# Performance work log

Hardware: AMD Instinct MI355X
Metric: run time of the kernel (lower is better)

## Reference

```python
import jax, jax.numpy as jnp
import numpy as np

H = 64  # hidden_size
IN = 1  # input_size
OUT = 7  # output_size
B, T = 4096, 512


def setup_inputs() -> dict:
    key = jax.random.key(0)
    ks = jax.random.split(key, 11)
    s = 1.0 / np.sqrt(H)  # PyTorch LSTM init scale
    u = lambda k, shp: jax.random.uniform(k, shp, jnp.float32, -s, s)
    return {
        "x": jax.random.normal(ks[0], (B, T, IN), jnp.float32),
        # layer 0
        "Wih0": u(ks[1], (4 * H, IN)),
        "Whh0": u(ks[2], (4 * H, H)),
        "bih0": u(ks[3], (4 * H,)),
        "bhh0": u(ks[4], (4 * H,)),
        # layer 1
        "Wih1": u(ks[5], (4 * H, H)),
        "Whh1": u(ks[6], (4 * H, H)),
        "bih1": u(ks[7], (4 * H,)),
        "bhh1": u(ks[8], (4 * H,)),
        # fc head
        "Wfc": u(ks[9], (OUT, H)),
        "bfc": u(ks[10], (OUT,)),
    }


def _lstm_layer(x, Wih, Whh, bih, bhh):
    """x: [B, T, F] -> hidden sequence [B, T, H]. PyTorch gate order i,f,g,o."""
    b, t, _ = x.shape
    h = Whh.shape[1]
    # precompute input contribution for all timesteps: [T, B, 4H]
    xg = (jnp.einsum('btf,gf->btg', x, Wih) + bih + bhh).transpose(1, 0, 2)
    WhhT = Whh.T  # [H, 4H]

    def step(carry, g_t):
        h_t, c_t = carry
        gates = g_t + h_t @ WhhT  # [B, 4H]
        i, f, g, o = jnp.split(gates, 4, axis=-1)
        i = jax.nn.sigmoid(i)
        f = jax.nn.sigmoid(f)
        g = jnp.tanh(g)
        o = jax.nn.sigmoid(o)
        c_new = f * c_t + i * g
        h_new = o * jnp.tanh(c_new)
        return (h_new, c_new), h_new

    h0 = jnp.zeros((b, h), x.dtype)
    c0 = jnp.zeros((b, h), x.dtype)
    (_, _), hs = jax.lax.scan(step, (h0, c0), xg)
    return hs.transpose(1, 0, 2)  # [B, T, H]


def reference(x, Wih0, Whh0, bih0, bhh0, Wih1, Whh1, bih1, bhh1, Wfc, bfc):
    h1 = _lstm_layer(x, Wih0, Whh0, bih0, bhh0)   # dropout between layers is identity in eval
    h2 = _lstm_layer(h1, Wih1, Whh1, bih1, bhh1)
    last = h2[:, -1, :]  # [B, H]; dropout identity in eval
    return last @ Wfc.T + bfc  # [B, OUT]
```

## Files before the change

kernel.cpp:

```cpp
#include <hip/hip_runtime.h>

#define HH 64
#define TT 512
#define BB 16

typedef __attribute__((ext_vector_type(8))) short short8;
typedef __attribute__((ext_vector_type(4))) float f32x4;

static __device__ __forceinline__ unsigned short f2bf(float f) {
  unsigned u = __float_as_uint(f);
  u += 0x7fffu + ((u >> 16) & 1u);
  return (unsigned short)(u >> 16);
}

static __device__ __forceinline__ float sigm(float x) {
  float e = __builtin_amdgcn_exp2f(-1.442695041f * x);
  return __builtin_amdgcn_rcpf(1.0f + e);
}
static __device__ __forceinline__ float tanh_fast(float x) {
  float e = __builtin_amdgcn_exp2f(2.885390082f * x);
  return 1.0f - 2.0f * __builtin_amdgcn_rcpf(1.0f + e);
}

static __device__ __forceinline__ short8 pack8(const float* __restrict__ p) {
  const float4* p4 = (const float4*)p;
  float4 a = p4[0], b = p4[1];
  short8 r;
  r[0] = (short)f2bf(a.x); r[1] = (short)f2bf(a.y);
  r[2] = (short)f2bf(a.z); r[3] = (short)f2bf(a.w);
  r[4] = (short)f2bf(b.x); r[5] = (short)f2bf(b.y);
  r[6] = (short)f2bf(b.z); r[7] = (short)f2bf(b.w);
  return r;
}

static __device__ __forceinline__ short8 ldfrag(const unsigned short* buf, int m, int q, int kt) {
  const int off = (kt * 64 + q * 16) ^ ((m & 7) << 4);
  return *(const short8*)((const char*)buf + m * 128 + off);
}

__global__ __launch_bounds__(512)
void lstm2_fused(const float* __restrict__ x,
                 const float* __restrict__ Wih0, const float* __restrict__ Whh0,
                 const float* __restrict__ bih0, const float* __restrict__ bhh0,
                 const float* __restrict__ Wih1, const float* __restrict__ Whh1,
                 const float* __restrict__ bih1, const float* __restrict__ bhh1,
                 const float* __restrict__ Wfc,  const float* __restrict__ bfc,
                 float* __restrict__ out)
{
  __shared__ float xs[TT * BB];
  __shared__ __align__(16) unsigned short h0buf[BB * HH];
  __shared__ __align__(16) unsigned short h1buf[BB * HH];
  __shared__ float h1f[BB * HH];

  const int tid  = threadIdx.x;
  const int wave = tid >> 6;
  const int lane = tid & 63;
  const int grp  = wave >> 2;
  const int w    = wave & 3;
  const int m    = lane & 15;
  const int q    = lane >> 4;
  const int b0   = blockIdx.x * BB;

  {
    const int t = tid;
    #pragma unroll
    for (int r = 0; r < BB; ++r)
      xs[t * BB + r] = x[(size_t)(b0 + r) * TT + t];
  }
  h0buf[tid] = 0; h0buf[tid + 512] = 0;
  h1buf[tid] = 0; h1buf[tid + 512] = 0;

  short8 wf[16];
  float bsum[4], wx[4];
  #pragma unroll
  for (int n = 0; n < 4; ++n) {
    const int colg = 16 * (4 * n + w) + m;
    if (grp == 0) {
      bsum[n] = bih0[colg] + bhh0[colg];
      wx[n]   = Wih0[colg];
      #pragma unroll
      for (int kt = 0; kt < 2; ++kt)
        wf[n * 2 + kt] = pack8(Whh0 + colg * HH + kt * 32 + q * 8);
    } else {
      bsum[n] = bih1[colg] + bhh1[colg];
      wx[n]   = 0.f;
      #pragma unroll
      for (int kt = 0; kt < 4; ++kt) {
        const float* Wsrc = (kt < 2) ? Wih1 : Whh1;
        wf[n * 4 + kt] = pack8(Wsrc + colg * HH + (kt & 1) * 32 + q * 8);
      }
    }
  }

  __syncthreads();

  float cst[4] = {0.f, 0.f, 0.f, 0.f};
  const int colw = 16 * w + m;

  for (int t = 0; t <= TT; ++t) {
    const bool actA = (grp == 0) && (t < TT);
    const bool actB = (grp == 1) && (t >= 1);
    short8 af0, af1, af2, af3;
    if (actA) {
      af0 = ldfrag(h0buf, m, q, 0);
      af1 = ldfrag(h0buf, m, q, 1);
    } else if (actB) {
      af0 = ldfrag(h0buf, m, q, 0);
      af1 = ldfrag(h0buf, m, q, 1);
      af2 = ldfrag(h1buf, m, q, 0);
      af3 = ldfrag(h1buf, m, q, 1);
    }
    __syncthreads();

    if (actA) {
      f32x4 acc[4];
      float xv[4];
      #pragma unroll
      for (int j = 0; j < 4; ++j) xv[j] = xs[t * BB + q * 4 + j];
      #pragma unroll
      for (int n = 0; n < 4; ++n) {
        #pragma unroll
        for (int j = 0; j < 4; ++j) acc[n][j] = fmaf(xv[j], wx[n], bsum[n]);
      }
      #pragma unroll
      for (int n = 0; n < 4; ++n) {
        acc[n] = __builtin_amdgcn_mfma_f32_16x16x32_bf16(af0, wf[n*2+0], acc[n], 0, 0, 0);
        acc[n] = __builtin_amdgcn_mfma_f32_16x16x32_bf16(af1, wf[n*2+1], acc[n], 0, 0, 0);
      }
      #pragma unroll
      for (int j = 0; j < 4; ++j) {
        float iv = sigm(acc[0][j]);
        float fv = sigm(acc[1][j]);
        float gv = tanh_fast(acc[2][j]);
        float ov = sigm(acc[3][j]);
        float c  = fmaf(fv, cst[j], iv * gv);
        cst[j] = c;
        float h  = ov * tanh_fast(c);
        const int row = q * 4 + j;
        const int off = (2 * colw) ^ ((row & 7) << 4);
        *(unsigned short*)((char*)h0buf + row * 128 + off) = f2bf(h);
      }
    } else if (actB) {
      f32x4 acc[4];
      #pragma unroll
      for (int n = 0; n < 4; ++n) {
        acc[n][0] = bsum[n]; acc[n][1] = bsum[n]; acc[n][2] = bsum[n]; acc[n][3] = bsum[n];
      }
      #pragma unroll
      for (int n = 0; n < 4; ++n) {
        acc[n] = __builtin_amdgcn_mfma_f32_16x16x32_bf16(af0, wf[n*4+0], acc[n], 0, 0, 0);
        acc[n] = __builtin_amdgcn_mfma_f32_16x16x32_bf16(af1, wf[n*4+1], acc[n], 0, 0, 0);
        acc[n] = __builtin_amdgcn_mfma_f32_16x16x32_bf16(af2, wf[n*4+2], acc[n], 0, 0, 0);
        acc[n] = __builtin_amdgcn_mfma_f32_16x16x32_bf16(af3, wf[n*4+3], acc[n], 0, 0, 0);
      }
      const bool last = (t == TT);
      #pragma unroll
      for (int j = 0; j < 4; ++j) {
        float iv = sigm(acc[0][j]);
        float fv = sigm(acc[1][j]);
        float gv = tanh_fast(acc[2][j]);
        float ov = sigm(acc[3][j]);
        float c  = fmaf(fv, cst[j], iv * gv);
        cst[j] = c;
        float h  = ov * tanh_fast(c);
        const int row = q * 4 + j;
        const int off = (2 * colw) ^ ((row & 7) << 4);
        *(unsigned short*)((char*)h1buf + row * 128 + off) = f2bf(h);
        if (last) h1f[row * HH + colw] = h;
      }
    }
    __syncthreads();
  }

  if (tid < BB * 7) {
    const int b = tid / 7, o = tid % 7;
    float s = bfc[o];
    #pragma unroll
    for (int k = 0; k < HH; ++k) s = fmaf(h1f[b * HH + k], Wfc[o * HH + k], s);
    out[(size_t)(b0 + b) * 7 + o] = s;
  }
}

extern "C" void kernel_launch(void* const* d_in, const int* in_sizes, int n_in,
                              void* d_out, int out_size, void* d_ws, size_t ws_size,
                              hipStream_t stream) {
  const float* x    = (const float*)d_in[0];
  const float* Wih0 = (const float*)d_in[1];
  const float* Whh0 = (const float*)d_in[2];
  const float* bih0 = (const float*)d_in[3];
  const float* bhh0 = (const float*)d_in[4];
  const float* Wih1 = (const float*)d_in[5];
  const float* Whh1 = (const float*)d_in[6];
  const float* bih1 = (const float*)d_in[7];
  const float* bhh1 = (const float*)d_in[8];
  const float* Wfc  = (const float*)d_in[9];
  const float* bfc  = (const float*)d_in[10];
  float* out = (float*)d_out;

  dim3 grid(4096 / BB);
  dim3 block(512);
  hipLaunchKernelGGL(lstm2_fused, grid, block, 0, stream,
                     x, Wih0, Whh0, bih0, bhh0, Wih1, Whh1, bih1, bhh1, Wfc, bfc, out);
}
```

Measured before the change: 421.8 us.

## Double the waves per block and double-buffer hidden state to drop a barrier

```diff
diff --git a/kernel.cpp b/kernel.cpp
--- a/kernel.cpp
+++ b/kernel.cpp
@@ -38,7 +38,7 @@
   return *(const short8*)((const char*)buf + m * 128 + off);
 }
 
-__global__ __launch_bounds__(512)
+__global__ __launch_bounds__(1024)
 void lstm2_fused(const float* __restrict__ x,
                  const float* __restrict__ Wih0, const float* __restrict__ Whh0,
                  const float* __restrict__ bih0, const float* __restrict__ bhh0,
@@ -48,27 +48,29 @@
                  float* __restrict__ out)
 {
   __shared__ float xs[TT * BB];
-  __shared__ __align__(16) unsigned short h0buf[BB * HH];
-  __shared__ __align__(16) unsigned short h1buf[BB * HH];
+  __shared__ __align__(16) unsigned short h0buf[2][BB * HH];
+  __shared__ __align__(16) unsigned short h1buf[2][BB * HH];
   __shared__ float h1f[BB * HH];
 
   const int tid  = threadIdx.x;
   const int wave = tid >> 6;
   const int lane = tid & 63;
-  const int grp  = wave >> 2;
-  const int w    = wave & 3;
+  const int grp  = wave >> 3;
+  const int sub  = wave & 7;
+  const int w    = sub >> 1;
+  const int jh   = sub & 1;
   const int m    = lane & 15;
   const int q    = lane >> 4;
   const int b0   = blockIdx.x * BB;
 
-  {
+  if (tid < TT) {
     const int t = tid;
     #pragma unroll
     for (int r = 0; r < BB; ++r)
       xs[t * BB + r] = x[(size_t)(b0 + r) * TT + t];
   }
-  h0buf[tid] = 0; h0buf[tid + 512] = 0;
-  h1buf[tid] = 0; h1buf[tid + 512] = 0;
+  h0buf[0][tid] = 0; h0buf[1][tid] = 0;
+  h1buf[0][tid] = 0; h1buf[1][tid] = 0;
 
   short8 wf[16];
   float bsum[4], wx[4];
@@ -94,33 +96,26 @@
 
   __syncthreads();
 
-  float cst[4] = {0.f, 0.f, 0.f, 0.f};
-  const int colw = 16 * w + m;
+  float cst[2] = {0.f, 0.f};
+  const int colw  = 16 * w + m;
+  const int jbase = 2 * jh;
 
   for (int t = 0; t <= TT; ++t) {
+    const int p = t & 1;
+    const unsigned short* h0rd = h0buf[p ^ 1];
+    const unsigned short* h1rd = h1buf[p];
+    unsigned short* h0wr = h0buf[p];
+    unsigned short* h1wr = h1buf[p ^ 1];
     const bool actA = (grp == 0) && (t < TT);
     const bool actB = (grp == 1) && (t >= 1);
-    short8 af0, af1, af2, af3;
+
     if (actA) {
-      af0 = ldfrag(h0buf, m, q, 0);
-      af1 = ldfrag(h0buf, m, q, 1);
-    } else if (actB) {
-      af0 = ldfrag(h0buf, m, q, 0);
-      af1 = ldfrag(h0buf, m, q, 1);
-      af2 = ldfrag(h1buf, m, q, 0);
-      af3 = ldfrag(h1buf, m, q, 1);
-    }
-    __syncthreads();
-
-    if (actA) {
+      short8 af0 = ldfrag(h0rd, m, q, 0);
+      short8 af1 = ldfrag(h0rd, m, q, 1);
       f32x4 acc[4];
-      float xv[4];
-      #pragma unroll
-      for (int j = 0; j < 4; ++j) xv[j] = xs[t * BB + q * 4 + j];
-      #pragma unroll
-      for (int n = 0; n < 4; ++n) {
-        #pragma unroll
-        for (int j = 0; j < 4; ++j) acc[n][j] = fmaf(xv[j], wx[n], bsum[n]);
+      #pragma unroll
+      for (int n = 0; n < 4; ++n) {
+        acc[n][0] = bsum[n]; acc[n][1] = bsum[n]; acc[n][2] = bsum[n]; acc[n][3] = bsum[n];
       }
       #pragma unroll
       for (int n = 0; n < 4; ++n) {
@@ -128,19 +123,32 @@
         acc[n] = __builtin_amdgcn_mfma_f32_16x16x32_bf16(af1, wf[n*2+1], acc[n], 0, 0, 0);
       }
       #pragma unroll
-      for (int j = 0; j < 4; ++j) {
-        float iv = sigm(acc[0][j]);
-        float fv = sigm(acc[1][j]);
-        float gv = tanh_fast(acc[2][j]);
-        float ov = sigm(acc[3][j]);
-        float c  = fmaf(fv, cst[j], iv * gv);
-        cst[j] = c;
+      for (int jj = 0; jj < 2; ++jj) {
+        float pi = jh ? acc[0][2 + jj] : acc[0][jj];
+        float pf = jh ? acc[1][2 + jj] : acc[1][jj];
+        float pg = jh ? acc[2][2 + jj] : acc[2][jj];
+        float po = jh ? acc[3][2 + jj] : acc[3][jj];
+        const float xv = xs[t * BB + q * 4 + jbase + jj];
+        pi = fmaf(xv, wx[0], pi);
+        pf = fmaf(xv, wx[1], pf);
+        pg = fmaf(xv, wx[2], pg);
+        po = fmaf(xv, wx[3], po);
+        float iv = sigm(pi);
+        float fv = sigm(pf);
+        float gv = tanh_fast(pg);
+        float ov = sigm(po);
+        float c  = fmaf(fv, cst[jj], iv * gv);
+        cst[jj] = c;
         float h  = ov * tanh_fast(c);
-        const int row = q * 4 + j;
+        const int row = q * 4 + jbase + jj;
         const int off = (2 * colw) ^ ((row & 7) << 4);
-        *(unsigned short*)((char*)h0buf + row * 128 + off) = f2bf(h);
+        *(unsigned short*)((char*)h0wr + row * 128 + off) = f2bf(h);
       }
     } else if (actB) {
+      short8 af0 = ldfrag(h0rd, m, q, 0);
+      short8 af1 = ldfrag(h0rd, m, q, 1);
+      short8 af2 = ldfrag(h1rd, m, q, 0);
+      short8 af3 = ldfrag(h1rd, m, q, 1);
       f32x4 acc[4];
       #pragma unroll
       for (int n = 0; n < 4; ++n) {
@@ -155,17 +163,21 @@
       }
       const bool last = (t == TT);
       #pragma unroll
-      for (int j = 0; j < 4; ++j) {
-        float iv = sigm(acc[0][j]);
-        float fv = sigm(acc[1][j]);
-        float gv = tanh_fast(acc[2][j]);
-        float ov = sigm(acc[3][j]);
-        float c  = fmaf(fv, cst[j], iv * gv);
-        cst[j] = c;
+      for (int jj = 0; jj < 2; ++jj) {
+        float pi = jh ? acc[0][2 + jj] : acc[0][jj];
+        float pf = jh ? acc[1][2 + jj] : acc[1][jj];
+        float pg = jh ? acc[2][2 + jj] : acc[2][jj];
+        float po = jh ? acc[3][2 + jj] : acc[3][jj];
+        float iv = sigm(pi);
+        float fv = sigm(pf);
+        float gv = tanh_fast(pg);
+        float ov = sigm(po);
+        float c  = fmaf(fv, cst[jj], iv * gv);
+        cst[jj] = c;
         float h  = ov * tanh_fast(c);
-        const int row = q * 4 + j;
+        const int row = q * 4 + jbase + jj;
         const int off = (2 * colw) ^ ((row & 7) << 4);
-        *(unsigned short*)((char*)h1buf + row * 128 + off) = f2bf(h);
+        *(unsigned short*)((char*)h1wr + row * 128 + off) = f2bf(h);
         if (last) h1f[row * HH + colw] = h;
       }
     }
@@ -198,7 +210,7 @@
   float* out = (float*)d_out;
 
   dim3 grid(4096 / BB);
-  dim3 block(512);
+  dim3 block(1024);
   hipLaunchKernelGGL(lstm2_fused, grid, block, 0, stream,
                      x, Wih0, Whh0, bih0, bhh0, Wih1, Whh1, bih1, bhh1, Wfc, bfc, out);
 }
```

Measured after the change: 500.7 us. +18.7%, slower.

## Double-buffer hidden states to drop one barrier per LSTM timestep

Applied to the files above, without the earlier changes.

```diff
diff --git a/kernel.cpp b/kernel.cpp
--- a/kernel.cpp
+++ b/kernel.cpp
@@ -1,4 +1,5 @@
 #include <hip/hip_runtime.h>
+#include <hip/hip_bf16.h>
 
 #define HH 64
 #define TT 512
@@ -33,12 +34,62 @@
   return r;
 }
 
-static __device__ __forceinline__ short8 ldfrag(const unsigned short* buf, int m, int q, int kt) {
-  const int off = (kt * 64 + q * 16) ^ ((m & 7) << 4);
-  return *(const short8*)((const char*)buf + m * 128 + off);
-}
-
-__global__ __launch_bounds__(512)
+#define MF(A, B, C) __builtin_amdgcn_mfma_f32_16x16x32_bf16((A), (B), (C), 0, 0, 0)
+
+#define STEP_A(P, XP) {                                                        \
+    const char* rd = (const char*)h0buf[(P) ^ 1];                              \
+    short8 af0 = *(const short8*)(rd + rdo0);                                  \
+    short8 af1 = *(const short8*)(rd + rdo1);                                  \
+    f32x4 xv = *(const f32x4*)(XP);                                            \
+    f32x4 a0 = MF(af0, wf[0], bs[0]); a0 = MF(af1, wf[1], a0);                 \
+    f32x4 a1 = MF(af0, wf[2], bs[1]); a1 = MF(af1, wf[3], a1);                 \
+    f32x4 a2 = MF(af0, wf[4], bs[2]); a2 = MF(af1, wf[5], a2);                 \
+    f32x4 a3 = MF(af0, wf[6], bs[3]); a3 = MF(af1, wf[7], a3);                 \
+    char* wrb = (char*)h0buf[P];                                               \
+    _Pragma("unroll")                                                          \
+    for (int j = 0; j < 4; ++j) {                                              \
+      float pi = fmaf(xv[j], wx[0], a0[j]);                                    \
+      float pf = fmaf(xv[j], wx[1], a1[j]);                                    \
+      float pg = fmaf(xv[j], wx[2], a2[j]);                                    \
+      float po = fmaf(xv[j], wx[3], a3[j]);                                    \
+      float iv = sigm(pi), fv = sigm(pf);                                      \
+      float gv = tanh_fast(pg), ov = sigm(po);                                 \
+      float c = fmaf(fv, cst[j], iv * gv);                                     \
+      cst[j] = c;                                                              \
+      float h = ov * tanh_fast(c);                                             \
+      *(__hip_bfloat16*)(wrb + wro[j]) = __float2bfloat16(h);                  \
+    }                                                                          \
+  }
+
+#define STEP_B(P, LAST) {                                                      \
+    const char* rd0 = (const char*)h0buf[(P) ^ 1];                             \
+    const char* rd1 = (const char*)h1buf[P];                                   \
+    short8 af0 = *(const short8*)(rd0 + rdo0);                                 \
+    short8 af1 = *(const short8*)(rd0 + rdo1);                                 \
+    short8 af2 = *(const short8*)(rd1 + rdo0);                                 \
+    short8 af3 = *(const short8*)(rd1 + rdo1);                                 \
+    f32x4 a0 = MF(af0, wf[0],  bs[0]); a0 = MF(af1, wf[1],  a0);               \
+    a0 = MF(af2, wf[2],  a0);  a0 = MF(af3, wf[3],  a0);                       \
+    f32x4 a1 = MF(af0, wf[4],  bs[1]); a1 = MF(af1, wf[5],  a1);               \
+    a1 = MF(af2, wf[6],  a1);  a1 = MF(af3, wf[7],  a1);                       \
+    f32x4 a2 = MF(af0, wf[8],  bs[2]); a2 = MF(af1, wf[9],  a2);               \
+    a2 = MF(af2, wf[10], a2);  a2 = MF(af3, wf[11], a2);                       \
+    f32x4 a3 = MF(af0, wf[12], bs[3]); a3 = MF(af1, wf[13], a3);               \
+    a3 = MF(af2, wf[14], a3);  a3 = MF(af3, wf[15], a3);                       \
+    char* wrb = (char*)h1buf[(P) ^ 1];                                         \
+    _Pragma("unroll")                                                          \
+    for (int j = 0; j < 4; ++j) {                                              \
+      float iv = sigm(a0[j]), fv = sigm(a1[j]);                                \
+      float gv = tanh_fast(a2[j]), ov = sigm(a3[j]);                           \
+      float c = fmaf(fv, cst[j], iv * gv);                                     \
+      cst[j] = c;                                                              \
+      float h = ov * tanh_fast(c);                                             \
+      *(__hip_bfloat16*)(wrb + wro[j]) = __float2bfloat16(h);                  \
+      if (LAST) h1f[(q * 4 + j) * HH + colw] = h;                              \
+    }                                                                          \
+  }
+
+__global__ __launch_bounds__(512, 2)
 void lstm2_fused(const float* __restrict__ x,
                  const float* __restrict__ Wih0, const float* __restrict__ Whh0,
                  const float* __restrict__ bih0, const float* __restrict__ bhh0,
@@ -48,8 +99,8 @@
                  float* __restrict__ out)
 {
   __shared__ float xs[TT * BB];
-  __shared__ __align__(16) unsigned short h0buf[BB * HH];
-  __shared__ __align__(16) unsigned short h1buf[BB * HH];
+  __shared__ __align__(16) unsigned short h0buf[2][BB * HH];
+  __shared__ __align__(16) unsigned short h1buf[2][BB * HH];
   __shared__ float h1f[BB * HH];
 
   const int tid  = threadIdx.x;
@@ -67,23 +118,26 @@
     for (int r = 0; r < BB; ++r)
       xs[t * BB + r] = x[(size_t)(b0 + r) * TT + t];
   }
-  h0buf[tid] = 0; h0buf[tid + 512] = 0;
-  h1buf[tid] = 0; h1buf[tid + 512] = 0;
+  ((unsigned int*)h0buf)[tid] = 0; ((unsigned int*)h0buf)[tid + 512] = 0;
+  ((unsigned int*)h1buf)[tid] = 0; ((unsigned int*)h1buf)[tid + 512] = 0;
 
   short8 wf[16];
-  float bsum[4], wx[4];
+  f32x4 bs[4];
+  float wx[4];
   #pragma unroll
   for (int n = 0; n < 4; ++n) {
     const int colg = 16 * (4 * n + w) + m;
     if (grp == 0) {
-      bsum[n] = bih0[colg] + bhh0[colg];
-      wx[n]   = Wih0[colg];
+      const float b = bih0[colg] + bhh0[colg];
+      bs[n][0] = b; bs[n][1] = b; bs[n][2] = b; bs[n][3] = b;
+      wx[n] = Wih0[colg];
       #pragma unroll
       for (int kt = 0; kt < 2; ++kt)
         wf[n * 2 + kt] = pack8(Whh0 + colg * HH + kt * 32 + q * 8);
     } else {
-      bsum[n] = bih1[colg] + bhh1[colg];
-      wx[n]   = 0.f;
+      const float b = bih1[colg] + bhh1[colg];
+      bs[n][0] = b; bs[n][1] = b; bs[n][2] = b; bs[n][3] = b;
+      wx[n] = 0.f;
       #pragma unroll
       for (int kt = 0; kt < 4; ++kt) {
         const float* Wsrc = (kt < 2) ? Wih1 : Whh1;
@@ -92,85 +146,38 @@
     }
   }
 
+  const int colw = 16 * w + m;
+  const int rdo0 = m * 128 + ((q * 16) ^ ((m & 7) << 4));
+  const int rdo1 = m * 128 + ((64 + q * 16) ^ ((m & 7) << 4));
+  int wro[4];
+  #pragma unroll
+  for (int j = 0; j < 4; ++j) {
+    const int row = q * 4 + j;
+    wro[j] = row * 128 + ((2 * colw) ^ ((row & 7) << 4));
+  }
+
   __syncthreads();
 
   float cst[4] = {0.f, 0.f, 0.f, 0.f};
-  const int colw = 16 * w + m;
-
-  for (int t = 0; t <= TT; ++t) {
-    const bool actA = (grp == 0) && (t < TT);
-    const bool actB = (grp == 1) && (t >= 1);
-    short8 af0, af1, af2, af3;
-    if (actA) {
-      af0 = ldfrag(h0buf, m, q, 0);
-      af1 = ldfrag(h0buf, m, q, 1);
-    } else if (actB) {
-      af0 = ldfrag(h0buf, m, q, 0);
-      af1 = ldfrag(h0buf, m, q, 1);
-      af2 = ldfrag(h1buf, m, q, 0);
-      af3 = ldfrag(h1buf, m, q, 1);
-    }
+  const float* xp = xs + q * 4;
+
+  if (grp == 0) { STEP_A(0, xp) }
+  xp += BB;
+  __syncthreads();
+
+  #pragma unroll 1
+  for (int k = 0; k < (TT - 2) / 2; ++k) {
+    if (grp == 0) { STEP_A(1, xp) } else { STEP_B(1, false) }
+    xp += BB;
     __syncthreads();
-
-    if (actA) {
-      f32x4 acc[4];
-      float xv[4];
-      #pragma unroll
-      for (int j = 0; j < 4; ++j) xv[j] = xs[t * BB + q * 4 + j];
-      #pragma unroll
-      for (int n = 0; n < 4; ++n) {
-        #pragma unroll
-        for (int j = 0; j < 4; ++j) acc[n][j] = fmaf(xv[j], wx[n], bsum[n]);
-      }
-      #pragma unroll
-      for (int n = 0; n < 4; ++n) {
-        acc[n] = __builtin_amdgcn_mfma_f32_16x16x32_bf16(af0, wf[n*2+0], acc[n], 0, 0, 0);
-        acc[n] = __builtin_amdgcn_mfma_f32_16x16x32_bf16(af1, wf[n*2+1], acc[n], 0, 0, 0);
-      }
-      #pragma unroll
-      for (int j = 0; j < 4; ++j) {
-        float iv = sigm(acc[0][j]);
-        float fv = sigm(acc[1][j]);
-        float gv = tanh_fast(acc[2][j]);
-        float ov = sigm(acc[3][j]);
-        float c  = fmaf(fv, cst[j], iv * gv);
-        cst[j] = c;
-        float h  = ov * tanh_fast(c);
-        const int row = q * 4 + j;
-        const int off = (2 * colw) ^ ((row & 7) << 4);
-        *(unsigned short*)((char*)h0buf + row * 128 + off) = f2bf(h);
-      }
-    } else if (actB) {
-      f32x4 acc[4];
-      #pragma unroll
-      for (int n = 0; n < 4; ++n) {
-        acc[n][0] = bsum[n]; acc[n][1] = bsum[n]; acc[n][2] = bsum[n]; acc[n][3] = bsum[n];
-      }
-      #pragma unroll
-      for (int n = 0; n < 4; ++n) {
-        acc[n] = __builtin_amdgcn_mfma_f32_16x16x32_bf16(af0, wf[n*4+0], acc[n], 0, 0, 0);
-        acc[n] = __builtin_amdgcn_mfma_f32_16x16x32_bf16(af1, wf[n*4+1], acc[n], 0, 0, 0);
-        acc[n] = __builtin_amdgcn_mfma_f32_16x16x32_bf16(af2, wf[n*4+2], acc[n], 0, 0, 0);
-        acc[n] = __builtin_amdgcn_mfma_f32_16x16x32_bf16(af3, wf[n*4+3], acc[n], 0, 0, 0);
-      }
-      const bool last = (t == TT);
-      #pragma unroll
-      for (int j = 0; j < 4; ++j) {
-        float iv = sigm(acc[0][j]);
-        float fv = sigm(acc[1][j]);
-        float gv = tanh_fast(acc[2][j]);
-        float ov = sigm(acc[3][j]);
-        float c  = fmaf(fv, cst[j], iv * gv);
-        cst[j] = c;
-        float h  = ov * tanh_fast(c);
-        const int row = q * 4 + j;
-        const int off = (2 * colw) ^ ((row & 7) << 4);
-        *(unsigned short*)((char*)h1buf + row * 128 + off) = f2bf(h);
-        if (last) h1f[row * HH + colw] = h;
-      }
-    }
+    if (grp == 0) { STEP_A(0, xp) } else { STEP_B(0, false) }
+    xp += BB;
     __syncthreads();
   }
+  if (grp == 0) { STEP_A(1, xp) } else { STEP_B(1, false) }
+  __syncthreads();
+  if (grp == 1) { STEP_B(0, true) }
+  __syncthreads();
 
   if (tid < BB * 7) {
     const int b = tid / 7, o = tid % 7;
```

After: 371.0 us. 12.1% less time.
